# Kernel optimization log

Measured on AMD Instinct MI355X. Metric: run time of the kernel, lower is better.

The kernel has to match this reference:

```python
import jax, jax.numpy as jnp
import numpy as np

K_MAX = 16
SCALE = 1.0 / (32 * 32)


def setup_inputs() -> dict:
    key = jax.random.key(0)
    k1, k2, k3 = jax.random.split(key, 3)
    B, C_in, C_out, H, W = 16, 32, 32, 256, 256
    x = jax.random.normal(k1, (B, C_in, H, W), dtype=jnp.float32)
    weights_real = SCALE * jax.random.normal(k2, (C_in, C_out, K_MAX, K_MAX), dtype=jnp.float32)
    weights_imag = SCALE * jax.random.normal(k3, (C_in, C_out, K_MAX, K_MAX), dtype=jnp.float32)
    return {"x": x, "weights_real": weights_real, "weights_imag": weights_imag}


def reference(x, weights_real, weights_imag):
    B, C, H, W = x.shape
    C_out = weights_real.shape[1]
    k = min(K_MAX, H, W // 2 + 1)
    x_ft = jnp.fft.rfft2(x, norm='ortho')                 # (B, C, H, W//2+1) complex64
    w = (weights_real + 1j * weights_imag)[:, :, :k, :k]  # (C, C_out, k, k)
    # Faithful to original einsum 'bijk,ijkm->bkm' with broadcast over the
    # size-1 i/j slices: sums x_ft over its ROW axis; x_ft's COLUMN index
    # becomes the output-block row index.
    S = jnp.sum(x_ft[:, :, :k, :k], axis=2)               # (B, C, k)  indexed by freq column
    blk = jnp.einsum('bir,iorc->borc', S, w)              # (B, C_out, k, k)
    out_ft = jnp.zeros((B, C_out, H, W // 2 + 1), dtype=x_ft.dtype)
    out_ft = out_ft.at[:, :, :k, :k].set(blk)
    return jnp.fft.irfft2(out_ft, s=(H, W), norm='ortho')
```

## Files before the change

### kernel.cpp

```cpp
#include <hip/hip_runtime.h>
#include <math.h>


#define TWO_PI_OVER_256 0.02454369260617026

__global__ __launch_bounds__(256) void k0_tables(float* __restrict__ tbl)
{
    const int t = threadIdx.x;
    const double a = TWO_PI_OVER_256 * (double)t;
    tbl[t]       = (float)cos(a);
    tbl[256 + t] = (float)sin(a);
}

__global__ __launch_bounds__(256) void k1_partial(
    const float* __restrict__ x, const float* __restrict__ tbl,
    float* __restrict__ s_part)
{
    __shared__ float twc[256], tws[256];
    __shared__ float gre[64], gim[64];
    __shared__ float Pre[4][256], Pim[4][256];
    __shared__ float red_re[16][16], red_im[16][16];

    const int t = threadIdx.x;
    const int blk = blockIdx.x;
    const int bi = blk >> 2, chunk = blk & 3;
    const int y0 = chunk << 6;

    twc[t] = tbl[t];
    tws[t] = tbl[256 + t];
    __syncthreads();
    if (t < 64) {
        const int h = y0 + t;
        float gr = 0.f, gi = 0.f;
        #pragma unroll
        for (int u = 0; u < 16; ++u) {
            const int idx = (u * h) & 255;
            gr += twc[idx];
            gi -= tws[idx];
        }
        gre[t] = gr; gim[t] = gi;
    }
    __syncthreads();

    const float* img = x + (size_t)bi * 65536 + (size_t)y0 * 256;
    const int cg = t & 63, rg = t >> 6;
    float4 pr = {0.f,0.f,0.f,0.f}, pi = {0.f,0.f,0.f,0.f};
    #pragma unroll 4
    for (int k = 0; k < 16; ++k) {
        const int hl = rg + (k << 2);
        const float4 xv = *(const float4*)(img + (hl << 8) + (cg << 2));
        const float gr = gre[hl], gi = gim[hl];
        pr.x += gr * xv.x; pr.y += gr * xv.y; pr.z += gr * xv.z; pr.w += gr * xv.w;
        pi.x += gi * xv.x; pi.y += gi * xv.y; pi.z += gi * xv.z; pi.w += gi * xv.w;
    }
    *(float4*)&Pre[rg][cg << 2] = pr;
    *(float4*)&Pim[rg][cg << 2] = pi;
    __syncthreads();

    {
        const int v = t >> 4, j = t & 15;
        float ar = 0.f, ai = 0.f;
        #pragma unroll
        for (int m = 0; m < 16; ++m) {
            const int w = j + (m << 4);
            const float prr = Pre[0][w] + Pre[1][w] + Pre[2][w] + Pre[3][w];
            const float pii = Pim[0][w] + Pim[1][w] + Pim[2][w] + Pim[3][w];
            const int idx = (v * w) & 255;
            const float c = twc[idx], s = tws[idx];
            ar += prr * c + pii * s;
            ai += pii * c - prr * s;
        }
        red_re[v][j] = ar; red_im[v][j] = ai;
    }
    __syncthreads();
    if (t < 16) {
        float ar = 0.f, ai = 0.f;
        #pragma unroll
        for (int j = 0; j < 16; ++j) { ar += red_re[t][j]; ai += red_im[t][j]; }
        float* sp = s_part + (size_t)bi * 128 + chunk * 32;
        sp[t]      = ar * (1.0f / 256.0f);
        sp[t + 16] = ai * (1.0f / 256.0f);
    }
}

__global__ __launch_bounds__(256) void k23_synth(
    const float* __restrict__ wr, const float* __restrict__ wi,
    const float* __restrict__ s_part, const float* __restrict__ tbl,
    float* __restrict__ out)
{
    __shared__ float twc[256], tws[256];
    __shared__ float Sre[32][16], Sim[32][16];
    __shared__ float Br[256], Bi[256];
    __shared__ __align__(16) float coef[64][36];

    const int t = threadIdx.x;
    const int blk = blockIdx.x;
    const int bo = blk >> 2;
    const int y0 = (blk & 3) << 6;
    const int b = bo >> 5, o = bo & 31;

    twc[t] = tbl[t];
    tws[t] = tbl[256 + t];
    {
        const float* sb = s_part + (size_t)b * 4096;
        #pragma unroll
        for (int e = t; e < 512; e += 256) {
            const int i = e >> 4, u = e & 15;
            const float* p = sb + i * 128 + u;
            Sre[i][u] = p[0] + p[32] + p[64] + p[96];
            Sim[i][u] = p[16] + p[48] + p[80] + p[112];
        }
    }
    __syncthreads();

    {
        const int u = t >> 4;
        float br = 0.f, bim = 0.f;
        const float* wrp = wr + o * 256 + t;
        const float* wip = wi + o * 256 + t;
        #pragma unroll 8
        for (int i = 0; i < 32; ++i) {
            const float a_re = Sre[i][u], a_im = Sim[i][u];
            const float w_re = wrp[i * 8192], w_im = wip[i * 8192];
            br  += a_re * w_re - a_im * w_im;
            bim += a_re * w_im + a_im * w_re;
        }
        Br[t] = br; Bi[t] = bim;
    }
    __syncthreads();

    {
        const int v = t & 15, slot = t >> 4;
        float br[16], bim[16];
        #pragma unroll
        for (int u = 0; u < 16; ++u) { br[u] = Br[u * 16 + v]; bim[u] = Bi[u * 16 + v]; }
        const float scale = (v == 0) ? (1.0f / 256.0f) : (1.0f / 128.0f);
        #pragma unroll
        for (int m = 0; m < 4; ++m) {
            const int r = slot * 4 + m;
            const int y = y0 + r;
            const float c1 = twc[y], s1 = tws[y];
            float gr = br[0], gi = bim[0];
            float cc = 1.f, cs = 0.f;
            #pragma unroll
            for (int u = 1; u < 16; ++u) {
                const float nc = cc * c1 - cs * s1;
                const float ns = cc * s1 + cs * c1;
                cc = nc; cs = ns;
                gr += br[u] * cc - bim[u] * cs;
                gi += br[u] * cs + bim[u] * cc;
            }
            coef[r][v]      = gr * scale;
            coef[r][16 + v] = (v == 0) ? 0.f : (-gi * scale);
        }
    }
    __syncthreads();

    const int c0 = t & 63, rg = t >> 6;
    float cv[16], sv[16];
    #pragma unroll
    for (int v = 0; v < 16; ++v) {
        const int idx = (v * c0) & 255;
        cv[v] = twc[idx];
        sv[v] = tws[idx];
    }
    sv[0] = 0.f;

#define PTERM(ACC, C_, S_, vv) ACC += (C_) * cv[vv] + (S_) * sv[vv];
#define QTERM(ACC, C_, S_, vv) ACC += (S_) * cv[vv] - (C_) * sv[vv];

    float* op = out + (size_t)bo * 65536 + (size_t)y0 * 256;
    #pragma unroll 2
    for (int rr = 0; rr < 16; ++rr) {
        const int r = (rg << 4) + rr;
        const float4* crow = (const float4*)&coef[r][0];
        const float4 pc0 = crow[0], pc1 = crow[1], pc2 = crow[2], pc3 = crow[3];
        const float4 ps0 = crow[4], ps1 = crow[5], ps2 = crow[6], ps3 = crow[7];
        float P0 = 0.f, P1 = 0.f, P2 = 0.f, P3 = 0.f, Q1 = 0.f, Q3 = 0.f;
        PTERM(P0, pc0.x, ps0.x, 0)
        PTERM(P1, pc0.y, ps0.y, 1)   QTERM(Q1, pc0.y, ps0.y, 1)
        PTERM(P2, pc0.z, ps0.z, 2)
        PTERM(P3, pc0.w, ps0.w, 3)   QTERM(Q3, pc0.w, ps0.w, 3)
        PTERM(P0, pc1.x, ps1.x, 4)
        PTERM(P1, pc1.y, ps1.y, 5)   QTERM(Q1, pc1.y, ps1.y, 5)
        PTERM(P2, pc1.z, ps1.z, 6)
        PTERM(P3, pc1.w, ps1.w, 7)   QTERM(Q3, pc1.w, ps1.w, 7)
        PTERM(P0, pc2.x, ps2.x, 8)
        PTERM(P1, pc2.y, ps2.y, 9)   QTERM(Q1, pc2.y, ps2.y, 9)
        PTERM(P2, pc2.z, ps2.z, 10)
        PTERM(P3, pc2.w, ps2.w, 11)  QTERM(Q3, pc2.w, ps2.w, 11)
        PTERM(P0, pc3.x, ps3.x, 12)
        PTERM(P1, pc3.y, ps3.y, 13)  QTERM(Q1, pc3.y, ps3.y, 13)
        PTERM(P2, pc3.z, ps3.z, 14)
        PTERM(P3, pc3.w, ps3.w, 15)  QTERM(Q3, pc3.w, ps3.w, 15)

        const float e02 = P0 + P2, o13 = P1 + P3;
        const float d02 = P0 - P2, dq  = Q1 - Q3;
        float* row = op + (r << 8) + c0;
        row[0]   = e02 + o13;
        row[64]  = d02 + dq;
        row[128] = e02 - o13;
        row[192] = d02 - dq;
    }
#undef PTERM
#undef QTERM
}

extern "C" void kernel_launch(void* const* d_in, const int* in_sizes, int n_in,
                              void* d_out, int out_size, void* d_ws, size_t ws_size,
                              hipStream_t stream) {
    (void)in_sizes; (void)n_in; (void)out_size; (void)ws_size;
    const float* x  = (const float*)d_in[0];
    const float* wr = (const float*)d_in[1];
    const float* wi = (const float*)d_in[2];
    float* out    = (float*)d_out;
    float* s_part = (float*)d_ws;
    float* tbl    = s_part + 65536;

    k0_tables<<<1, 256, 0, stream>>>(tbl);
    k1_partial<<<2048, 256, 0, stream>>>(x, tbl, s_part);
    k23_synth<<<2048, 256, 0, stream>>>(wr, wi, s_part, tbl, out);
}
```

Baseline: 259.2 us.

## Split synthesis kernel into coefficient and output-writing kernels via global buffer

The fused synthesis kernel is split in two. The first kernel computes per-row coefficients and writes them to a global workspace buffer. The second reads those coefficients with uniform (readfirstlane) addressing and writes the output image without shared memory or barriers. The aim is a lean, store-bound write kernel with less LDS and fewer syncs, at the cost of an extra launch and a global round trip for the coefficients.

Measured after the change: 268.4 us. 3.6% more time.

```diff
diff --git a/kernel.cpp b/kernel.cpp
--- a/kernel.cpp
+++ b/kernel.cpp
@@ -83,15 +83,13 @@
     }
 }
 
-__global__ __launch_bounds__(256) void k23_synth(
+__global__ __launch_bounds__(256) void k2_coef(
     const float* __restrict__ wr, const float* __restrict__ wi,
     const float* __restrict__ s_part, const float* __restrict__ tbl,
-    float* __restrict__ out)
-{
-    __shared__ float twc[256], tws[256];
+    float* __restrict__ coef_g)
+{
     __shared__ float Sre[32][16], Sim[32][16];
     __shared__ float Br[256], Bi[256];
-    __shared__ __align__(16) float coef[64][36];
 
     const int t = threadIdx.x;
     const int blk = blockIdx.x;
@@ -99,8 +97,6 @@
     const int y0 = (blk & 3) << 6;
     const int b = bo >> 5, o = bo & 31;
 
-    twc[t] = tbl[t];
-    tws[t] = tbl[256 + t];
     {
         const float* sb = s_part + (size_t)b * 4096;
         #pragma unroll
@@ -135,11 +131,12 @@
         #pragma unroll
         for (int u = 0; u < 16; ++u) { br[u] = Br[u * 16 + v]; bim[u] = Bi[u * 16 + v]; }
         const float scale = (v == 0) ? (1.0f / 256.0f) : (1.0f / 128.0f);
+        float* cg = coef_g + (size_t)bo * 8192 + (size_t)y0 * 32;
         #pragma unroll
         for (int m = 0; m < 4; ++m) {
             const int r = slot * 4 + m;
             const int y = y0 + r;
-            const float c1 = twc[y], s1 = tws[y];
+            const float c1 = tbl[y], s1 = tbl[256 + y];
             float gr = br[0], gi = bim[0];
             float cc = 1.f, cs = 0.f;
             #pragma unroll
@@ -150,30 +147,41 @@
                 gr += br[u] * cc - bim[u] * cs;
                 gi += br[u] * cs + bim[u] * cc;
             }
-            coef[r][v]      = gr * scale;
-            coef[r][16 + v] = (v == 0) ? 0.f : (-gi * scale);
-        }
-    }
-    __syncthreads();
-
-    const int c0 = t & 63, rg = t >> 6;
+            cg[r * 32 + v]      = gr * scale;
+            cg[r * 32 + 16 + v] = (v == 0) ? 0.f : (-gi * scale);
+        }
+    }
+}
+
+__global__ __launch_bounds__(256) void k3_synth(
+    const float* __restrict__ coef_g, const float* __restrict__ tbl,
+    float* __restrict__ out)
+{
+    const int t = threadIdx.x;
+    const int blk = blockIdx.x;
+    const int bo = blk >> 2;
+    const int y0 = (blk & 3) << 6;
+    const int c0 = t & 63;
+    const int rg = __builtin_amdgcn_readfirstlane(t >> 6);
+
     float cv[16], sv[16];
     #pragma unroll
     for (int v = 0; v < 16; ++v) {
         const int idx = (v * c0) & 255;
-        cv[v] = twc[idx];
-        sv[v] = tws[idx];
+        cv[v] = tbl[idx];
+        sv[v] = tbl[256 + idx];
     }
     sv[0] = 0.f;
 
 #define PTERM(ACC, C_, S_, vv) ACC += (C_) * cv[vv] + (S_) * sv[vv];
 #define QTERM(ACC, C_, S_, vv) ACC += (S_) * cv[vv] - (C_) * sv[vv];
 
-    float* op = out + (size_t)bo * 65536 + (size_t)y0 * 256;
-    #pragma unroll 2
+    const float* crow_base = coef_g + (size_t)bo * 8192 + (size_t)(y0 + rg * 16) * 32;
+    float* op = out + (size_t)bo * 65536 + (size_t)(y0 + rg * 16) * 256 + c0;
+
+    #pragma unroll 4
     for (int rr = 0; rr < 16; ++rr) {
-        const int r = (rg << 4) + rr;
-        const float4* crow = (const float4*)&coef[r][0];
+        const float4* crow = (const float4*)(crow_base + rr * 32);
         const float4 pc0 = crow[0], pc1 = crow[1], pc2 = crow[2], pc3 = crow[3];
         const float4 ps0 = crow[4], ps1 = crow[5], ps2 = crow[6], ps3 = crow[7];
         float P0 = 0.f, P1 = 0.f, P2 = 0.f, P3 = 0.f, Q1 = 0.f, Q3 = 0.f;
@@ -196,7 +204,7 @@
 
         const float e02 = P0 + P2, o13 = P1 + P3;
         const float d02 = P0 - P2, dq  = Q1 - Q3;
-        float* row = op + (r << 8) + c0;
+        float* row = op + (rr << 8);
         row[0]   = e02 + o13;
         row[64]  = d02 + dq;
         row[128] = e02 - o13;
@@ -216,8 +224,10 @@
     float* out    = (float*)d_out;
     float* s_part = (float*)d_ws;
     float* tbl    = s_part + 65536;
+    float* coef_g = tbl + 512;
 
     k0_tables<<<1, 256, 0, stream>>>(tbl);
     k1_partial<<<2048, 256, 0, stream>>>(x, tbl, s_part);
-    k23_synth<<<2048, 256, 0, stream>>>(wr, wi, s_part, tbl, out);
-}
+    k2_coef<<<2048, 256, 0, stream>>>(wr, wi, s_part, tbl, coef_g);
+    k3_synth<<<2048, 256, 0, stream>>>(coef_g, tbl, out);
+}
```
